# Performance work log

Measured on AMD Instinct MI355X. Metric: run time of the kernel, lower is better.

## Reference

```python
import jax, jax.numpy as jnp
import numpy as np

N_NODES = 50000


def gcn_layer(x, src, dst, ew, W, b, n_nodes):
    # PyG GCNConv: add self-loops (weight 1), symmetric deg^-1/2 normalization,
    # linear transform, scatter-add aggregation at destination, then bias.
    loop = jnp.arange(n_nodes, dtype=src.dtype)
    s = jnp.concatenate([src, loop])
    d = jnp.concatenate([dst, loop])
    w = jnp.concatenate([ew, jnp.ones((n_nodes,), dtype=ew.dtype)])
    deg = jax.ops.segment_sum(w, d, num_segments=n_nodes)  # [N]
    dinv = jnp.where(deg > 0, jax.lax.rsqrt(jnp.where(deg > 0, deg, 1.0)), 0.0)
    norm = dinv[s] * w * dinv[d]  # [E+N]
    h = x @ W  # [N, out]
    msg = h[s] * norm[:, None]  # gather + scale, [E+N, out]
    out = jax.ops.segment_sum(msg, d, num_segments=n_nodes)  # scatter-add
    return out + b


def setup_inputs() -> dict:
    key = jax.random.key(0)
    k1, k2, k3, k4, k5, k6, k7 = jax.random.split(key, 7)
    N, E, C_IN, C_OUT = N_NODES, 600000, 128, 128
    x = jax.random.normal(k1, (N, C_IN), dtype=jnp.float32)
    edge_index = jax.random.randint(k2, (2, E), 0, N, dtype=jnp.int64)
    edge_weight = jax.random.uniform(k3, (E,), dtype=jnp.float32)
    # Glorot-style init like PyG's Linear default
    s1 = 1.0 / np.sqrt(C_IN)
    s2 = 1.0 / np.sqrt(C_OUT)
    W1 = jax.random.uniform(k4, (C_IN, C_OUT), jnp.float32, -s1, s1)
    b1 = jnp.zeros((C_OUT,), dtype=jnp.float32)
    W2 = jax.random.uniform(k5, (C_OUT, C_OUT), jnp.float32, -s2, s2)
    b2 = jnp.zeros((C_OUT,), dtype=jnp.float32)
    return {"x": x, "edge_index": edge_index, "edge_weight": edge_weight,
            "W1": W1, "b1": b1, "W2": W2, "b2": b2}


def reference(x, edge_index, edge_weight, W1, b1, W2, b2):
    src, dst = edge_index[0], edge_index[1]
    h = jax.nn.relu(gcn_layer(x, src, dst, edge_weight, W1, b1, N_NODES))
    return jax.nn.relu(gcn_layer(h, src, dst, edge_weight, W2, b2, N_NODES))
```

## Files before the change

kernel.cpp:

```cpp
#include <hip/hip_runtime.h>
#include <math.h>

#define CH   128
#define CH4  32
#define TPB  256
#define SCANB 1024
#define WIMG 16384
#define NREP 8

typedef __attribute__((ext_vector_type(8))) short short8;
typedef __attribute__((ext_vector_type(4))) float floatx4;
typedef __attribute__((ext_vector_type(8))) float float8;

static __device__ __forceinline__ unsigned short f2bf(float f) {
    unsigned u = __float_as_uint(f);
    return (unsigned short)((u + 0x7fffu + ((u >> 16) & 1u)) >> 16);
}
static __device__ __forceinline__ float bf2f(unsigned short s) {
    return __uint_as_float(((unsigned)s) << 16);
}
static __device__ __forceinline__ float8 bf8_to_f8(short8 u) {
    float8 f;
    #pragma unroll
    for (int i = 0; i < 8; ++i) f[i] = bf2f((unsigned short)u[i]);
    return f;
}

__global__ void k_prep(const float* __restrict__ W1, const float* __restrict__ W2,
                       short* __restrict__ Wsplit) {
    int i = blockIdx.x * blockDim.x + threadIdx.x;
    if (i >= 2 * CH * CH) return;
    int layer = i >> 14;
    int idx   = i & 16383;
    int k = idx >> 7, c = idx & 127;
    float w = (layer ? W2 : W1)[k * CH + c];
    unsigned short hi = f2bf(w);
    unsigned short lo = f2bf(w - bf2f(hi));
    int colh = c >> 6, nn = c & 63;
    int kt = k >> 5, q = (k & 31) >> 3, j = k & 7;
    int ns = nn >> 4, ln = q * 16 + (nn & 15);
    size_t base = (size_t)(layer * 2 + colh) * WIMG;
    size_t off  = ((size_t)(kt * 4 + ns) * 64 + ln) * 8 + j;
    Wsplit[base + off]        = (short)hi;
    Wsplit[base + 8192 + off] = (short)lo;
}

static __device__ __forceinline__ void gemm_body_f32(
        const float* __restrict__ X, const short* __restrict__ Wfrag,
        unsigned short* __restrict__ H, int n, int tile, int colh, int tid) {
    __shared__ __align__(16) short sW[2][4][4][64][8];
    {
        const float4* gsrc = (const float4*)Wfrag;
        float4* ldst = (float4*)sW;
        #pragma unroll
        for (int i = 0; i < 8; ++i)
            ldst[i * TPB + tid] = gsrc[i * TPB + tid];
    }
    __syncthreads();

    const int lane = tid & 63;
    const int wv   = tid >> 6;
    const int q    = lane >> 4;
    const int m    = lane & 15;
    const int row0 = tile * 64 + wv * 16;
    if (row0 >= n) return;

    int rrow = row0 + m;
    if (rrow > n - 1) rrow = n - 1;

    const float4* xr = (const float4*)(X + (size_t)rrow * CH);
    float4 xa[4][2];
    #pragma unroll
    for (int kt = 0; kt < 4; ++kt) {
        xa[kt][0] = xr[kt * 8 + q * 2 + 0];
        xa[kt][1] = xr[kt * 8 + q * 2 + 1];
    }

    floatx4 acc[4];
    #pragma unroll
    for (int ns = 0; ns < 4; ++ns) acc[ns] = (floatx4){0.f, 0.f, 0.f, 0.f};

    #pragma unroll
    for (int kt = 0; kt < 4; ++kt) {
        float xf[8] = { xa[kt][0].x, xa[kt][0].y, xa[kt][0].z, xa[kt][0].w,
                        xa[kt][1].x, xa[kt][1].y, xa[kt][1].z, xa[kt][1].w };
        short8 ah, al;
        #pragma unroll
        for (int j = 0; j < 8; ++j) {
            float v = xf[j];
            unsigned short h = f2bf(v);
            ah[j] = (short)h;
            al[j] = (short)f2bf(v - bf2f(h));
        }
        #pragma unroll
        for (int ns = 0; ns < 4; ++ns) {
            short8 bh = *(const short8*)&sW[0][kt][ns][lane][0];
            short8 bl = *(const short8*)&sW[1][kt][ns][lane][0];
            acc[ns] = __builtin_amdgcn_mfma_f32_16x16x32_bf16(ah, bh, acc[ns], 0, 0, 0);
            acc[ns] = __builtin_amdgcn_mfma_f32_16x16x32_bf16(al, bh, acc[ns], 0, 0, 0);
            acc[ns] = __builtin_amdgcn_mfma_f32_16x16x32_bf16(ah, bl, acc[ns], 0, 0, 0);
        }
    }

    #pragma unroll
    for (int ns = 0; ns < 4; ++ns) {
        #pragma unroll
        for (int reg = 0; reg < 4; ++reg) {
            int r = row0 + q * 4 + reg;
            if (r < n)
                H[(size_t)r * CH + colh * 64 + ns * 16 + m] = f2bf(acc[ns][reg]);
        }
    }
}

__global__ __launch_bounds__(TPB, 4)
void k_gemm_rank(const float* __restrict__ X, const short* __restrict__ Wsplit,
                 unsigned short* __restrict__ H, int n,
                 const int* __restrict__ dst, int* __restrict__ counts_rep,
                 int* __restrict__ rank, int E, int nbE4, int Np) {
    int bx = blockIdx.x;
    if (bx < nbE4) {
        int stride = nbE4 * TPB;
        int e = bx * TPB + threadIdx.x;
        #pragma unroll
        for (int it = 0; it < 4; ++it, e += stride) {
            if (e < E) {
                int d = dst[e];
                if ((unsigned)d < (unsigned)n) {
                    int rep = e & (NREP - 1);
                    rank[e] = atomicAdd(&counts_rep[rep * Np + d], 1);
                }
            }
        }
    } else {
        bx -= nbE4;
        int colh = bx & 1;
        gemm_body_f32(X, Wsplit + (size_t)colh * WIMG, H, n, bx >> 1, colh,
                      threadIdx.x);
    }
}

__global__ __launch_bounds__(TPB, 4)
void k_gemm_bf(const unsigned short* __restrict__ X, const short* __restrict__ Wsplit,
               unsigned short* __restrict__ H, int n) {
    __shared__ __align__(16) short sW[4][4][64][8];
    const int tid  = threadIdx.x;
    const int colh = (int)blockIdx.x & 1;
    const int tile = (int)blockIdx.x >> 1;
    {
        const float4* gsrc = (const float4*)(Wsplit + (size_t)colh * WIMG);
        float4* ldst = (float4*)sW;
        #pragma unroll
        for (int i = 0; i < 4; ++i)
            ldst[i * TPB + tid] = gsrc[i * TPB + tid];
    }
    __syncthreads();

    const int lane = tid & 63;
    const int wv   = tid >> 6;
    const int q    = lane >> 4;
    const int m    = lane & 15;
    const int row0 = tile * 64 + wv * 16;
    if (row0 >= n) return;

    int rrow = row0 + m;
    if (rrow > n - 1) rrow = n - 1;

    const short8* xr8 = (const short8*)(X + (size_t)rrow * CH);
    short8 a[4];
    #pragma unroll
    for (int kt = 0; kt < 4; ++kt) a[kt] = xr8[kt * 4 + q];

    floatx4 acc[4];
    #pragma unroll
    for (int ns = 0; ns < 4; ++ns) acc[ns] = (floatx4){0.f, 0.f, 0.f, 0.f};

    #pragma unroll
    for (int kt = 0; kt < 4; ++kt) {
        #pragma unroll
        for (int ns = 0; ns < 4; ++ns) {
            short8 bh = *(const short8*)&sW[kt][ns][lane][0];
            acc[ns] = __builtin_amdgcn_mfma_f32_16x16x32_bf16(a[kt], bh, acc[ns], 0, 0, 0);
        }
    }

    #pragma unroll
    for (int ns = 0; ns < 4; ++ns) {
        #pragma unroll
        for (int reg = 0; reg < 4; ++reg) {
            int r = row0 + q * 4 + reg;
            if (r < n)
                H[(size_t)r * CH + colh * 64 + ns * 16 + m] = f2bf(acc[ns][reg]);
        }
    }
}

__global__ __launch_bounds__(SCANB)
void k_scan1(const int* __restrict__ counts_rep, int Np,
             int* __restrict__ counts_tot, int* __restrict__ repoff8,
             int* __restrict__ row_start, int* __restrict__ partials,
             int* __restrict__ pp_s, int* __restrict__ done, int nb, int n) {
    __shared__ int s[SCANB];
    __shared__ int slast;
    int gid = blockIdx.x * SCANB + threadIdx.x;
    int c[NREP];
    int v = 0;
    #pragma unroll
    for (int r = 0; r < NREP; ++r) {
        c[r] = (gid < n) ? counts_rep[r * Np + gid] : 0;
        v += c[r];
    }
    s[threadIdx.x] = v;
    __syncthreads();
    for (int off = 1; off < SCANB; off <<= 1) {
        int t = (threadIdx.x >= off) ? s[threadIdx.x - off] : 0;
        __syncthreads();
        s[threadIdx.x] += t;
        __syncthreads();
    }
    if (gid < n) {
        row_start[gid]  = s[threadIdx.x] - v;
        counts_tot[gid] = v;
        int pre = 0;
        int ro[NREP];
        #pragma unroll
        for (int r = 0; r < NREP; ++r) { ro[r] = pre; pre += c[r]; }
        ((int4*)repoff8)[gid * 2 + 0] = make_int4(ro[0], ro[1], ro[2], ro[3]);
        ((int4*)repoff8)[gid * 2 + 1] = make_int4(ro[4], ro[5], ro[6], ro[7]);
    }
    if (threadIdx.x == SCANB - 1) {
        partials[blockIdx.x] = s[SCANB - 1];
        __threadfence();
        int old = atomicAdd(done, 1);
        slast = (old == nb - 1);
    }
    __syncthreads();
    if (slast && threadIdx.x < 64) {
        int pv = (threadIdx.x < nb) ? atomicAdd(&partials[threadIdx.x], 0) : 0;
        int inc = pv;
        #pragma unroll
        for (int off = 1; off < 64; off <<= 1) {
            int t = __shfl_up(inc, off, 64);
            if ((threadIdx.x & 63) >= off) inc += t;
        }
        if (threadIdx.x < nb) pp_s[threadIdx.x] = inc - pv;
    }
}

__global__ void k_fill(const int* __restrict__ src, const int* __restrict__ dst,
                       const float* __restrict__ ew, const int* __restrict__ row_start,
                       const int* __restrict__ pp_s, const int* __restrict__ repoff8,
                       const int* __restrict__ rank, int2* __restrict__ edges,
                       int E, int n) {
    int e = blockIdx.x * blockDim.x + threadIdx.x;
    if (e >= E) return;
    int s = src[e], d = dst[e];
    if ((unsigned)s >= (unsigned)n || (unsigned)d >= (unsigned)n) return;
    int rep = e & (NREP - 1);
    int base = row_start[d] + pp_s[d >> 10] + repoff8[d * NREP + rep];
    edges[base + rank[e]] = make_int2(s, __float_as_int(ew[e]));
}

__global__ void k_deg(const int* __restrict__ row_start, const int* __restrict__ pp_s,
                      const int* __restrict__ counts, const int2* __restrict__ edges,
                      float* __restrict__ dinv, int n) {
    int i = blockIdx.x * blockDim.x + threadIdx.x;
    if (i >= n) return;
    int j = row_start[i] + pp_s[i >> 10], end = j + counts[i];
    float sum = 1.0f;
    for (; j < end; ++j) sum += __int_as_float(edges[j].y);
    dinv[i] = rsqrtf(sum);
}

template<int FIXUP>
static __device__ __forceinline__ float8 agg_node8(
        const short8* __restrict__ h8, int2* __restrict__ edges,
        const float* __restrict__ dinv, const float8 b, int node, int tx,
        const int* __restrict__ row_start, const int* __restrict__ pp_s,
        const int* __restrict__ counts) {
    float di = dinv[node];
    float8 hv = bf8_to_f8(h8[(size_t)node * 16 + tx]);
    float8 acc;
    #pragma unroll
    for (int i = 0; i < 8; ++i) acc[i] = 0.f;

    int j   = row_start[node] + pp_s[node >> 10];
    int end = j + counts[node];

    for (; j + 8 <= end; j += 8) {
        int2 e[8];
        #pragma unroll
        for (int i = 0; i < 8; ++i) e[i] = edges[j + i];
        short8 g[8];
        #pragma unroll
        for (int i = 0; i < 8; ++i) g[i] = h8[(size_t)e[i].x * 16 + tx];
        float w[8];
        #pragma unroll
        for (int i = 0; i < 8; ++i) {
            w[i] = __int_as_float(e[i].y);
            if (FIXUP) w[i] *= dinv[e[i].x];
        }
        if (FIXUP && tx == 0) {
            #pragma unroll
            for (int i = 0; i < 8; ++i) edges[j + i].y = __float_as_int(w[i]);
        }
        #pragma unroll
        for (int i = 0; i < 8; ++i) {
            float8 gf = bf8_to_f8(g[i]);
            #pragma unroll
            for (int c = 0; c < 8; ++c) acc[c] += gf[c] * w[i];
        }
    }
    if (j + 4 <= end) {
        int2 e[4];
        #pragma unroll
        for (int i = 0; i < 4; ++i) e[i] = edges[j + i];
        short8 g[4];
        #pragma unroll
        for (int i = 0; i < 4; ++i) g[i] = h8[(size_t)e[i].x * 16 + tx];
        float w[4];
        #pragma unroll
        for (int i = 0; i < 4; ++i) {
            w[i] = __int_as_float(e[i].y);
            if (FIXUP) w[i] *= dinv[e[i].x];
        }
        if (FIXUP && tx == 0) {
            #pragma unroll
            for (int i = 0; i < 4; ++i) edges[j + i].y = __float_as_int(w[i]);
        }
        #pragma unroll
        for (int i = 0; i < 4; ++i) {
            float8 gf = bf8_to_f8(g[i]);
            #pragma unroll
            for (int c = 0; c < 8; ++c) acc[c] += gf[c] * w[i];
        }
        j += 4;
    }
    for (; j < end; ++j) {
        int2 e0 = edges[j];
        float w0 = __int_as_float(e0.y);
        if (FIXUP) w0 *= dinv[e0.x];
        if (FIXUP && tx == 0) edges[j].y = __float_as_int(w0);
        float8 gf = bf8_to_f8(h8[(size_t)e0.x * 16 + tx]);
        #pragma unroll
        for (int c = 0; c < 8; ++c) acc[c] += gf[c] * w0;
    }

    float sc = di * di;
    float8 o;
    #pragma unroll
    for (int c = 0; c < 8; ++c) o[c] = hv[c] * sc + b[c] + di * acc[c];
    return o;
}

__global__ __launch_bounds__(TPB)
void k_aggregate1(const unsigned short* __restrict__ h,
                  const int* __restrict__ row_start, const int* __restrict__ pp_s,
                  const int* __restrict__ counts, int2* __restrict__ edges,
                  const float* __restrict__ dinv, const float* __restrict__ bias,
                  unsigned short* __restrict__ out, int n) {
    int t = blockIdx.x * blockDim.x + threadIdx.x;
    int node = t >> 4;
    if (node >= n) return;
    int tx = t & 15;
    float8 b;
    #pragma unroll
    for (int c = 0; c < 8; ++c) b[c] = bias[tx * 8 + c];
    float8 o = agg_node8<1>((const short8*)h, edges, dinv, b, node, tx,
                            row_start, pp_s, counts);
    short8 u;
    #pragma unroll
    for (int c = 0; c < 8; ++c) u[c] = (short)f2bf(fmaxf(o[c], 0.f));
    ((short8*)out)[(size_t)node * 16 + tx] = u;
}

__global__ __launch_bounds__(TPB)
void k_aggregate2(const unsigned short* __restrict__ h,
                  const int* __restrict__ row_start, const int* __restrict__ pp_s,
                  const int* __restrict__ counts, int2* __restrict__ edges,
                  const float* __restrict__ dinv, const float* __restrict__ bias,
                  float* __restrict__ out, int n) {
    int t = blockIdx.x * blockDim.x + threadIdx.x;
    int node = t >> 4;
    if (node >= n) return;
    int tx = t & 15;
    float8 b;
    #pragma unroll
    for (int c = 0; c < 8; ++c) b[c] = bias[tx * 8 + c];
    float8 o = agg_node8<0>((const short8*)h, edges, dinv, b, node, tx,
                            row_start, pp_s, counts);
    float4 lo = make_float4(fmaxf(o[0], 0.f), fmaxf(o[1], 0.f),
                            fmaxf(o[2], 0.f), fmaxf(o[3], 0.f));
    float4 hi = make_float4(fmaxf(o[4], 0.f), fmaxf(o[5], 0.f),
                            fmaxf(o[6], 0.f), fmaxf(o[7], 0.f));
    ((float4*)out)[(size_t)node * CH4 + tx * 2 + 0] = lo;
    ((float4*)out)[(size_t)node * CH4 + tx * 2 + 1] = hi;
}

extern "C" void kernel_launch(void* const* d_in, const int* in_sizes, int n_in,
                              void* d_out, int out_size, void* d_ws, size_t ws_size,
                              hipStream_t stream) {
    const float* x  = (const float*)d_in[0];
    const int*   ei = (const int*)d_in[1];
    const float* ew = (const float*)d_in[2];
    const float* W1 = (const float*)d_in[3];
    const float* b1 = (const float*)d_in[4];
    const float* W2 = (const float*)d_in[5];
    const float* b2 = (const float*)d_in[6];
    float* out = (float*)d_out;

    const int N = in_sizes[0] / CH;
    const int E = in_sizes[2];
    const int* src = ei;
    const int* dst = ei + E;

    size_t Np = ((size_t)N + 255) & ~(size_t)255;
    size_t Ep = ((size_t)E + 63) & ~(size_t)63;
    float* ws          = (float*)d_ws;
    float* dinv        = ws;
    unsigned short* h  = (unsigned short*)(dinv + Np);
    unsigned short* o1 = h + (size_t)N * CH;
    unsigned short* h2 = o1 + (size_t)N * CH;
    int*   counts_rep  = (int*)(h2 + (size_t)N * CH);
    int*   done        = counts_rep + NREP * Np;
    size_t zero_bytes  = (size_t)NREP * Np * 4 + 256;
    int*  counts_tot   = done + 64;
    int*  row_start    = counts_tot + Np;
    int*  repoff8      = row_start + Np;
    int*  rank         = repoff8 + NREP * Np;
    int*  partials     = rank + Ep;
    int*  pp_s         = partials + 64;
    int2* edges        = (int2*)(pp_s + 64);
    short* Wsplit      = (short*)(edges + E);

    const int nbN    = (N + TPB - 1) / TPB;
    const int nbE    = (E + TPB - 1) / TPB;
    const int nbE4   = (E + TPB * 4 - 1) / (TPB * 4);
    const int nbAgg  = (int)(((size_t)N * 16 + TPB - 1) / TPB);
    const int nbScan = (N + SCANB - 1) / SCANB;
    const int nbGemm2 = 2 * ((N + 63) / 64);
    const int nbPrep  = (2 * CH * CH + TPB - 1) / TPB;

    hipMemsetAsync(counts_rep, 0, zero_bytes, stream);
    k_prep     <<<nbPrep, TPB, 0, stream>>>(W1, W2, Wsplit);

    k_gemm_rank<<<nbE4 + nbGemm2, TPB, 0, stream>>>(x, Wsplit, h, N, dst,
                                                    counts_rep, rank, E, nbE4, (int)Np);
    k_scan1    <<<nbScan, SCANB, 0, stream>>>(counts_rep, (int)Np, counts_tot,
                                              repoff8, row_start, partials,
                                              pp_s, done, nbScan, N);
    k_fill     <<<nbE, TPB, 0, stream>>>(src, dst, ew, row_start, pp_s, repoff8,
                                         rank, edges, E, N);
    k_deg      <<<nbN, TPB, 0, stream>>>(row_start, pp_s, counts_tot, edges,
                                         dinv, N);

    k_aggregate1<<<nbAgg, TPB, 0, stream>>>(h, row_start, pp_s, counts_tot,
                                            edges, dinv, b1, o1, N);
    k_gemm_bf   <<<nbGemm2, TPB, 0, stream>>>(o1, Wsplit + 2 * (size_t)WIMG, h2, N);
    k_aggregate2<<<nbAgg, TPB, 0, stream>>>(h2, row_start, pp_s, counts_tot,
                                            edges, dinv, b2, out, N);
}
```

Baseline: 215.7 us.

## Prescale H rows by dinv instead of per-edge source normalization in aggregation

Moves the source-side deg^-1/2 factor out of the aggregation loop. After degree computation the layer-1 H rows are rescaled in place, and the layer-2 GEMM epilogue multiplies by dinv. This removes the per-edge dinv gather and the edge-weight write-back from aggregate1. The degree kernel now uses 16 lanes per node with a shuffle reduction, and the memset is folded into the prep kernel launch. It adds an extra bf16 round-trip on H, which slightly changes rounding.

```diff
diff --git a/kernel.cpp b/kernel.cpp
--- a/kernel.cpp
+++ b/kernel.cpp
@@ -27,8 +27,15 @@
 }
 
 __global__ void k_prep(const float* __restrict__ W1, const float* __restrict__ W2,
-                       short* __restrict__ Wsplit) {
-    int i = blockIdx.x * blockDim.x + threadIdx.x;
+                       short* __restrict__ Wsplit, float4* __restrict__ zbase,
+                       int nzero4, int nbPrep) {
+    int bx = blockIdx.x;
+    if (bx >= nbPrep) {
+        int i = (bx - nbPrep) * TPB + threadIdx.x;
+        if (i < nzero4) zbase[i] = make_float4(0.f, 0.f, 0.f, 0.f);
+        return;
+    }
+    int i = bx * TPB + threadIdx.x;
     if (i >= 2 * CH * CH) return;
     int layer = i >> 14;
     int idx   = i & 16383;
@@ -142,7 +149,7 @@
 
 __global__ __launch_bounds__(TPB, 4)
 void k_gemm_bf(const unsigned short* __restrict__ X, const short* __restrict__ Wsplit,
-               unsigned short* __restrict__ H, int n) {
+               const float* __restrict__ dinv, unsigned short* __restrict__ H, int n) {
     __shared__ __align__(16) short sW[4][4][64][8];
     const int tid  = threadIdx.x;
     const int colh = (int)blockIdx.x & 1;
@@ -184,13 +191,20 @@
         }
     }
 
+    float dr[4];
+    #pragma unroll
+    for (int reg = 0; reg < 4; ++reg) {
+        int r = row0 + q * 4 + reg;
+        dr[reg] = (r < n) ? dinv[r] : 0.f;
+    }
     #pragma unroll
     for (int ns = 0; ns < 4; ++ns) {
         #pragma unroll
         for (int reg = 0; reg < 4; ++reg) {
             int r = row0 + q * 4 + reg;
             if (r < n)
-                H[(size_t)r * CH + colh * 64 + ns * 16 + m] = f2bf(acc[ns][reg]);
+                H[(size_t)r * CH + colh * 64 + ns * 16 + m] =
+                    f2bf(acc[ns][reg] * dr[reg]);
         }
     }
 }
@@ -261,24 +275,37 @@
     edges[base + rank[e]] = make_int2(s, __float_as_int(ew[e]));
 }
 
-__global__ void k_deg(const int* __restrict__ row_start, const int* __restrict__ pp_s,
-                      const int* __restrict__ counts, const int2* __restrict__ edges,
-                      float* __restrict__ dinv, int n) {
-    int i = blockIdx.x * blockDim.x + threadIdx.x;
-    if (i >= n) return;
-    int j = row_start[i] + pp_s[i >> 10], end = j + counts[i];
-    float sum = 1.0f;
-    for (; j < end; ++j) sum += __int_as_float(edges[j].y);
-    dinv[i] = rsqrtf(sum);
-}
-
-template<int FIXUP>
+__global__ __launch_bounds__(TPB)
+void k_deg_scale(const int* __restrict__ row_start, const int* __restrict__ pp_s,
+                 const int* __restrict__ counts, const int2* __restrict__ edges,
+                 float* __restrict__ dinv, unsigned short* __restrict__ h, int n) {
+    int t = blockIdx.x * blockDim.x + threadIdx.x;
+    int node = t >> 4;
+    if (node >= n) return;
+    int tx = t & 15;
+    int j0  = row_start[node] + pp_s[node >> 10];
+    int cnt = counts[node];
+    float sum = 0.f;
+    for (int j = tx; j < cnt; j += 16)
+        sum += __int_as_float(edges[j0 + j].y);
+    #pragma unroll
+    for (int off = 8; off; off >>= 1) sum += __shfl_down(sum, off, 16);
+    float di = rsqrtf(1.0f + __shfl(sum, 0, 16));
+    if (tx == 0) dinv[node] = di;
+    short8* hp = (short8*)h + (size_t)node * 16 + tx;
+    short8 v = *hp;
+    short8 o;
+    #pragma unroll
+    for (int c = 0; c < 8; ++c)
+        o[c] = (short)f2bf(bf2f((unsigned short)v[c]) * di);
+    *hp = o;
+}
+
 static __device__ __forceinline__ float8 agg_node8(
-        const short8* __restrict__ h8, int2* __restrict__ edges,
-        const float* __restrict__ dinv, const float8 b, int node, int tx,
+        const short8* __restrict__ h8, const int2* __restrict__ edges,
+        float di, const float8 b, int node, int tx,
         const int* __restrict__ row_start, const int* __restrict__ pp_s,
         const int* __restrict__ counts) {
-    float di = dinv[node];
     float8 hv = bf8_to_f8(h8[(size_t)node * 16 + tx]);
     float8 acc;
     #pragma unroll
@@ -294,21 +321,12 @@
         short8 g[8];
         #pragma unroll
         for (int i = 0; i < 8; ++i) g[i] = h8[(size_t)e[i].x * 16 + tx];
-        float w[8];
         #pragma unroll
         for (int i = 0; i < 8; ++i) {
-            w[i] = __int_as_float(e[i].y);
-            if (FIXUP) w[i] *= dinv[e[i].x];
-        }
-        if (FIXUP && tx == 0) {
-            #pragma unroll
-            for (int i = 0; i < 8; ++i) edges[j + i].y = __float_as_int(w[i]);
-        }
-        #pragma unroll
-        for (int i = 0; i < 8; ++i) {
+            float w = __int_as_float(e[i].y);
             float8 gf = bf8_to_f8(g[i]);
             #pragma unroll
-            for (int c = 0; c < 8; ++c) acc[c] += gf[c] * w[i];
+            for (int c = 0; c < 8; ++c) acc[c] += gf[c] * w;
         }
     }
     if (j + 4 <= end) {
@@ -318,45 +336,33 @@
         short8 g[4];
         #pragma unroll
         for (int i = 0; i < 4; ++i) g[i] = h8[(size_t)e[i].x * 16 + tx];
-        float w[4];
         #pragma unroll
         for (int i = 0; i < 4; ++i) {
-            w[i] = __int_as_float(e[i].y);
-            if (FIXUP) w[i] *= dinv[e[i].x];
-        }
-        if (FIXUP && tx == 0) {
-            #pragma unroll
-            for (int i = 0; i < 4; ++i) edges[j + i].y = __float_as_int(w[i]);
-        }
-        #pragma unroll
-        for (int i = 0; i < 4; ++i) {
+            float w = __int_as_float(e[i].y);
             float8 gf = bf8_to_f8(g[i]);
             #pragma unroll
-            for (int c = 0; c < 8; ++c) acc[c] += gf[c] * w[i];
+            for (int c = 0; c < 8; ++c) acc[c] += gf[c] * w;
         }
         j += 4;
     }
     for (; j < end; ++j) {
         int2 e0 = edges[j];
         float w0 = __int_as_float(e0.y);
-        if (FIXUP) w0 *= dinv[e0.x];
-        if (FIXUP && tx == 0) edges[j].y = __float_as_int(w0);
         float8 gf = bf8_to_f8(h8[(size_t)e0.x * 16 + tx]);
         #pragma unroll
         for (int c = 0; c < 8; ++c) acc[c] += gf[c] * w0;
     }
 
-    float sc = di * di;
     float8 o;
     #pragma unroll
-    for (int c = 0; c < 8; ++c) o[c] = hv[c] * sc + b[c] + di * acc[c];
+    for (int c = 0; c < 8; ++c) o[c] = di * (hv[c] + acc[c]) + b[c];
     return o;
 }
 
 __global__ __launch_bounds__(TPB)
 void k_aggregate1(const unsigned short* __restrict__ h,
                   const int* __restrict__ row_start, const int* __restrict__ pp_s,
-                  const int* __restrict__ counts, int2* __restrict__ edges,
+                  const int* __restrict__ counts, const int2* __restrict__ edges,
                   const float* __restrict__ dinv, const float* __restrict__ bias,
                   unsigned short* __restrict__ out, int n) {
     int t = blockIdx.x * blockDim.x + threadIdx.x;
@@ -366,8 +372,8 @@
     float8 b;
     #pragma unroll
     for (int c = 0; c < 8; ++c) b[c] = bias[tx * 8 + c];
-    float8 o = agg_node8<1>((const short8*)h, edges, dinv, b, node, tx,
-                            row_start, pp_s, counts);
+    float8 o = agg_node8((const short8*)h, edges, dinv[node], b, node, tx,
+                         row_start, pp_s, counts);
     short8 u;
     #pragma unroll
     for (int c = 0; c < 8; ++c) u[c] = (short)f2bf(fmaxf(o[c], 0.f));
@@ -377,7 +383,7 @@
 __global__ __launch_bounds__(TPB)
 void k_aggregate2(const unsigned short* __restrict__ h,
                   const int* __restrict__ row_start, const int* __restrict__ pp_s,
-                  const int* __restrict__ counts, int2* __restrict__ edges,
+                  const int* __restrict__ counts, const int2* __restrict__ edges,
                   const float* __restrict__ dinv, const float* __restrict__ bias,
                   float* __restrict__ out, int n) {
     int t = blockIdx.x * blockDim.x + threadIdx.x;
@@ -387,8 +393,8 @@
     float8 b;
     #pragma unroll
     for (int c = 0; c < 8; ++c) b[c] = bias[tx * 8 + c];
-    float8 o = agg_node8<0>((const short8*)h, edges, dinv, b, node, tx,
-                            row_start, pp_s, counts);
+    float8 o = agg_node8((const short8*)h, edges, dinv[node], b, node, tx,
+                         row_start, pp_s, counts);
     float4 lo = make_float4(fmaxf(o[0], 0.f), fmaxf(o[1], 0.f),
                             fmaxf(o[2], 0.f), fmaxf(o[3], 0.f));
     float4 hi = make_float4(fmaxf(o[4], 0.f), fmaxf(o[5], 0.f),
@@ -423,7 +429,7 @@
     unsigned short* h2 = o1 + (size_t)N * CH;
     int*   counts_rep  = (int*)(h2 + (size_t)N * CH);
     int*   done        = counts_rep + NREP * Np;
-    size_t zero_bytes  = (size_t)NREP * Np * 4 + 256;
+    int    nzero4      = (int)((NREP * Np + 64) / 4);
     int*  counts_tot   = done + 64;
     int*  row_start    = counts_tot + Np;
     int*  repoff8      = row_start + Np;
@@ -433,16 +439,17 @@
     int2* edges        = (int2*)(pp_s + 64);
     short* Wsplit      = (short*)(edges + E);
 
-    const int nbN    = (N + TPB - 1) / TPB;
     const int nbE    = (E + TPB - 1) / TPB;
     const int nbE4   = (E + TPB * 4 - 1) / (TPB * 4);
     const int nbAgg  = (int)(((size_t)N * 16 + TPB - 1) / TPB);
     const int nbScan = (N + SCANB - 1) / SCANB;
     const int nbGemm2 = 2 * ((N + 63) / 64);
     const int nbPrep  = (2 * CH * CH + TPB - 1) / TPB;
-
-    hipMemsetAsync(counts_rep, 0, zero_bytes, stream);
-    k_prep     <<<nbPrep, TPB, 0, stream>>>(W1, W2, Wsplit);
+    const int nbZero  = (nzero4 + TPB - 1) / TPB;
+
+    k_prep     <<<nbPrep + nbZero, TPB, 0, stream>>>(W1, W2, Wsplit,
+                                                     (float4*)counts_rep,
+                                                     nzero4, nbPrep);
 
     k_gemm_rank<<<nbE4 + nbGemm2, TPB, 0, stream>>>(x, Wsplit, h, N, dst,
                                                     counts_rep, rank, E, nbE4, (int)Np);
@@ -451,12 +458,13 @@
                                               pp_s, done, nbScan, N);
     k_fill     <<<nbE, TPB, 0, stream>>>(src, dst, ew, row_start, pp_s, repoff8,
                                          rank, edges, E, N);
-    k_deg      <<<nbN, TPB, 0, stream>>>(row_start, pp_s, counts_tot, edges,
-                                         dinv, N);
+    k_deg_scale<<<nbAgg, TPB, 0, stream>>>(row_start, pp_s, counts_tot, edges,
+                                           dinv, h, N);
 
     k_aggregate1<<<nbAgg, TPB, 0, stream>>>(h, row_start, pp_s, counts_tot,
                                             edges, dinv, b1, o1, N);
-    k_gemm_bf   <<<nbGemm2, TPB, 0, stream>>>(o1, Wsplit + 2 * (size_t)WIMG, h2, N);
+    k_gemm_bf   <<<nbGemm2, TPB, 0, stream>>>(o1, Wsplit + 2 * (size_t)WIMG,
+                                              dinv, h2, N);
     k_aggregate2<<<nbAgg, TPB, 0, stream>>>(h2, row_start, pp_s, counts_tot,
                                             edges, dinv, b2, out, N);
 }
```

After: 212.4 us. No clear change (-1.5%).
